# Kernel optimization log

Hardware: AMD Instinct MI355X
Metric: run time of the kernel (lower is better)

Reference implementation:

```python
import jax, jax.numpy as jnp
import numpy as np

C = 128          # channels per irrep
N = 16000        # nodes (atoms)
E = 256000       # edges (neighbour pairs)
A = 10           # node attribute (species) dim, '10x0e'
RB = 8           # radial basis features
H = 64           # radial MLP hidden width
INV_SQRT3 = 0.5773502691896258  # normalised CG for 1o x 1o -> 0e


def setup_inputs() -> dict:
    key = jax.random.key(0)
    ks = jax.random.split(key, 16)
    s = lambda fan: 1.0  # weights ~ N(0,1); e3nn-style 1/sqrt(fan_in) applied in forward
    return {
        "node_features": jax.random.normal(ks[0], (N, 4 * C), jnp.float32),   # [N, 128x0e + 128x1o]
        "node_attributes": jax.random.uniform(ks[1], (N, A), jnp.float32),
        "sph_harmonics": jax.random.normal(ks[2], (E, 4), jnp.float32),        # [E, 0e(1)+1o(3)]
        "radial_basis": jax.random.normal(ks[3], (E, RB), jnp.float32),
        "edge_index": jax.random.randint(ks[4], (2, E), 0, N),                 # [senders; receivers]
        # pre_linear (per-irrep channel mixing)
        "Wpre0": jax.random.normal(ks[5], (C, C), jnp.float32),
        "Wpre1": jax.random.normal(ks[6], (C, C), jnp.float32),
        # radial MLP 8 -> 64 -> 64 -> weight_numel(=4*C), no bias
        "Wm1": jax.random.normal(ks[7], (RB, H), jnp.float32),
        "Wm2": jax.random.normal(ks[8], (H, H), jnp.float32),
        "Wm3": jax.random.normal(ks[9], (H, 4 * C), jnp.float32),
        # post_linear: mid irreps 256x0e + 256x1o -> 128x0e + 128x1o
        "Wpost0": jax.random.normal(ks[10], (2 * C, C), jnp.float32),
        "Wpost1": jax.random.normal(ks[11], (2 * C, C), jnp.float32),
        # attribute mixer: FullyConnectedTensorProduct(features_out, '10x0e', features_out)
        "Wa0": jax.random.normal(ks[12], (C, A, C), jnp.float32),
        "Wa1": jax.random.normal(ks[13], (C, A, C), jnp.float32),
    }


def reference(node_features, node_attributes, sph_harmonics, radial_basis, edge_index,
              Wpre0, Wpre1, Wm1, Wm2, Wm3, Wpost0, Wpost1, Wa0, Wa1):
    n = node_features.shape[0]
    inv_c = 1.0 / np.sqrt(C).astype(np.float32)
    inv_2c = 1.0 / np.sqrt(2 * C).astype(np.float32)
    inv_ca = 1.0 / np.sqrt(C * A).astype(np.float32)

    # split e3nn-layout features: scalars [N,C], vectors [N,C,3]
    x0 = node_features[:, :C]
    x1 = node_features[:, C:].reshape(n, C, 3)

    # pre_linear (o3.Linear: per-irrep channel mix, 1/sqrt(fan_in))
    h0 = (x0 @ Wpre0) * inv_c
    h1 = jnp.einsum('nud,uw->nwd', x1, Wpre1) * inv_c

    snd, rcv = edge_index[0], edge_index[1]
    e0 = h0[snd]            # [E,C]   gather neighbour scalars
    e1 = h1[snd]            # [E,C,3] gather neighbour vectors
    Y0 = sph_harmonics[:, :1]   # [E,1]
    Y1 = sph_harmonics[:, 1:]   # [E,3]

    # per-edge TP weights from radial MLP (SiLU, no bias)
    hmlp = jax.nn.silu(radial_basis @ Wm1)
    hmlp = jax.nn.silu(hmlp @ Wm2)
    w = (hmlp @ Wm3).reshape(-1, 4, C)  # [E,4,C], one weight per (path, channel)

    # channel-wise (uvu) tensor product, CG-sparse paths:
    m0a = w[:, 0] * e0 * Y0                                              # 0e x 0e -> 0e
    m0b = w[:, 1] * jnp.einsum('ecd,ed->ec', e1, Y1) * INV_SQRT3         # 1o x 1o -> 0e
    m1a = w[:, 2][:, :, None] * e0[:, :, None] * Y1[:, None, :]          # 0e x 1o -> 1o
    m1b = w[:, 3][:, :, None] * e1 * Y0[:, :, None]                      # 1o x 0e -> 1o

    M0 = jnp.concatenate([m0a, m0b], axis=1)   # [E,2C]  mid 256x0e
    M1 = jnp.concatenate([m1a, m1b], axis=1)   # [E,2C,3] mid 256x1o

    # scatter-sum aggregation onto receiving nodes
    A0 = jax.ops.segment_sum(M0, rcv, num_segments=n)
    A1 = jax.ops.segment_sum(M1, rcv, num_segments=n)

    # post_linear: 256x0e+256x1o -> 128x0e+128x1o
    o0 = (A0 @ Wpost0) * inv_2c
    o1 = jnp.einsum('nud,uw->nwd', A1, Wpost1) * inv_2c

    # attribute mixer: FCTP with '10x0e' (scalars mix channels per irrep)
    a0 = jnp.einsum('nu,nv,uvw->nw', o0, node_attributes, Wa0) * inv_ca
    a1 = jnp.einsum('nud,nv,uvw->nwd', o1, node_attributes, Wa1) * inv_ca

    # UnflattenIrreps: [N, channels, irreps_dim] with dims 0e(1)+1o(3)
    return jnp.concatenate([a0[:, :, None], a1], axis=2)  # [N, C, 4]
```

## Files before the change

### kernel.cpp

```cpp
#include <hip/hip_runtime.h>
#include <hip/hip_bf16.h>

#define NN 16000
#define CC 128
#define EE 256000
#define AA 10

typedef short short8_t __attribute__((ext_vector_type(8)));
typedef float f32x4 __attribute__((ext_vector_type(4)));
typedef unsigned short u16x4 __attribute__((ext_vector_type(4)));

__device__ __forceinline__ float silu_f(float x) {
    return x / (1.0f + __expf(-x));
}

__device__ __forceinline__ float bf2f(unsigned short u) {
    unsigned int x = ((unsigned int)u) << 16;
    float f;
    __builtin_memcpy(&f, &x, 4);
    return f;
}

__device__ __forceinline__ unsigned short f2bf(float f) {
    __hip_bfloat16 b = __float2bfloat16(f);
    unsigned short u;
    __builtin_memcpy(&u, &b, 2);
    return u;
}

__global__ __launch_bounds__(256) void pre_kernel(const float* __restrict__ nf,
                                                  const float* __restrict__ Wpre0,
                                                  const float* __restrict__ Wpre1,
                                                  float4* __restrict__ h4) {
    __shared__ float4 lx[2][CC];
    const int c = threadIdx.x & 127;
    const int sub = threadIdx.x >> 7;
    const float inv_c = 0.08838834764831843f;
    const int n = blockIdx.x * 2 + sub;
    const float* row = nf + (size_t)n * 512;
    lx[sub][c] = make_float4(row[c], row[128 + 3 * c], row[128 + 3 * c + 1], row[128 + 3 * c + 2]);
    __syncthreads();
    float4 acc = make_float4(0.f, 0.f, 0.f, 0.f);
    #pragma unroll 8
    for (int u = 0; u < 128; ++u) {
        const float w0 = Wpre0[u * 128 + c];
        const float w1 = Wpre1[u * 128 + c];
        const float4 xv = lx[sub][u];
        acc.x += w0 * xv.x;
        acc.y += w1 * xv.y;
        acc.z += w1 * xv.z;
        acc.w += w1 * xv.w;
    }
    acc.x *= inv_c; acc.y *= inv_c; acc.z *= inv_c; acc.w *= inv_c;
    h4[(size_t)n * 128 + c] = acc;
}

__global__ __launch_bounds__(256) void count_kernel(const int* __restrict__ ei,
                                                    int* __restrict__ cnt) {
    const int e = blockIdx.x * 256 + threadIdx.x;
    if (e < EE) atomicAdd(&cnt[ei[EE + e]], 1);
}

__global__ __launch_bounds__(1024) void scan_kernel(const int* __restrict__ cnt,
                                                    int* __restrict__ cur) {
    __shared__ int part[1024];
    const int t = threadIdx.x;
    const int base = t * 16;
    int local[16];
    int s = 0;
    #pragma unroll
    for (int i = 0; i < 16; ++i) {
        const int idx = base + i;
        const int v = (idx < NN) ? cnt[idx] : 0;
        local[i] = s;
        s += v;
    }
    part[t] = s;
    __syncthreads();
    for (int off = 1; off < 1024; off <<= 1) {
        int v = (t >= off) ? part[t - off] : 0;
        __syncthreads();
        part[t] += v;
        __syncthreads();
    }
    const int pre = (t == 0) ? 0 : part[t - 1];
    #pragma unroll
    for (int i = 0; i < 16; ++i) {
        const int idx = base + i;
        if (idx < NN) cur[idx] = pre + local[i];
    }
}

__global__ __launch_bounds__(256) void fill_kernel(const int* __restrict__ ei,
                                                   int* __restrict__ cur,
                                                   int* __restrict__ perm) {
    const int e = blockIdx.x * 256 + threadIdx.x;
    if (e < EE) {
        const int r = ei[EE + e];
        const int pos = atomicAdd(&cur[r], 1);
        perm[pos] = e;
    }
}

__global__ __launch_bounds__(256) void gather_kernel(const int* __restrict__ perm,
                                                     const int* __restrict__ ei,
                                                     const float4* __restrict__ sph4,
                                                     int* __restrict__ ss,
                                                     int* __restrict__ rs,
                                                     float4* __restrict__ Ys) {
    const int e = blockIdx.x * 256 + threadIdx.x;
    const int p = perm[e];
    ss[e] = ei[p];
    rs[e] = ei[EE + p];
    Ys[e] = sph4[p];
}

__global__ __launch_bounds__(256) void mlp_kernel(const float* __restrict__ rb,
                                                  const float* __restrict__ Wm1,
                                                  const float* __restrict__ Wm2,
                                                  const int* __restrict__ perm,
                                                  unsigned short* __restrict__ hmS) {
    __shared__ float4 sW1[8][16];
    __shared__ float4 sW2[64][16];
    __shared__ unsigned short sH[256][64];
    const int tid = threadIdx.x;
    for (int i = tid; i < 8 * 16; i += 256) ((float4*)sW1)[i] = ((const float4*)Wm1)[i];
    for (int i = tid; i < 64 * 16; i += 256) ((float4*)sW2)[i] = ((const float4*)Wm2)[i];
    __syncthreads();
    const int e = blockIdx.x * 256 + tid;
    const int p = perm[e];
    const float4* rb4 = (const float4*)(rb + (size_t)p * 8);
    const float4 r0 = rb4[0], r1 = rb4[1];
    float r[8] = {r0.x, r0.y, r0.z, r0.w, r1.x, r1.y, r1.z, r1.w};
    float h1[64];
    #pragma unroll
    for (int o4 = 0; o4 < 16; ++o4) {
        float4 a = make_float4(0.f, 0.f, 0.f, 0.f);
        #pragma unroll
        for (int k = 0; k < 8; ++k) {
            const float4 wv = sW1[k][o4];
            a.x += r[k] * wv.x; a.y += r[k] * wv.y; a.z += r[k] * wv.z; a.w += r[k] * wv.w;
        }
        h1[o4 * 4 + 0] = silu_f(a.x);
        h1[o4 * 4 + 1] = silu_f(a.y);
        h1[o4 * 4 + 2] = silu_f(a.z);
        h1[o4 * 4 + 3] = silu_f(a.w);
    }
    #pragma unroll
    for (int o4 = 0; o4 < 16; ++o4) {
        float4 a = make_float4(0.f, 0.f, 0.f, 0.f);
        #pragma unroll 8
        for (int k = 0; k < 64; ++k) {
            const float4 wv = sW2[k][o4];
            a.x += h1[k] * wv.x; a.y += h1[k] * wv.y; a.z += h1[k] * wv.z; a.w += h1[k] * wv.w;
        }
        sH[tid][o4 * 4 + 0] = f2bf(silu_f(a.x));
        sH[tid][o4 * 4 + 1] = f2bf(silu_f(a.y));
        sH[tid][o4 * 4 + 2] = f2bf(silu_f(a.z));
        sH[tid][o4 * 4 + 3] = f2bf(silu_f(a.w));
    }
    __syncthreads();
    uint4* g4 = (uint4*)(hmS + (size_t)blockIdx.x * 256 * 64);
    const uint4* s4 = (const uint4*)sH;
    for (int i = tid; i < 2048; i += 256) g4[i] = s4[i];
}

__global__ __launch_bounds__(256) void w3t_kernel(const float* __restrict__ Wm3,
                                                  unsigned short* __restrict__ W3Thi,
                                                  unsigned short* __restrict__ W3Tlo) {
    const int idx = blockIdx.x * 256 + threadIdx.x;
    const int col = idx >> 6, k = idx & 63;
    const float v = Wm3[k * 512 + col];
    const unsigned short hi = f2bf(v);
    W3Thi[idx] = hi;
    W3Tlo[idx] = f2bf(v - bf2f(hi));
}

__global__ __launch_bounds__(512) void wmsgm_kernel(const unsigned short* __restrict__ hmS,
                                                    const unsigned short* __restrict__ W3Thi,
                                                    const unsigned short* __restrict__ W3Tlo,
                                                    const int* __restrict__ ss,
                                                    const int* __restrict__ rs,
                                                    const float4* __restrict__ Ys,
                                                    const float4* __restrict__ h4,
                                                    float* __restrict__ Acat) {
    __shared__ int lss[64];
    __shared__ int lrs[64];
    __shared__ float4 lY[64];
    const int tid = threadIdx.x;
    const int ebase = blockIdx.x * 64;
    if (tid < 64) {
        lss[tid] = ss[ebase + tid];
        lrs[tid] = rs[ebase + tid];
        lY[tid] = Ys[ebase + tid];
    }
    const int w = tid >> 6, lane = tid & 63;
    const int l15 = lane & 15, lk = lane >> 4;

    f32x4 acc[4][4];
    #pragma unroll
    for (int mf = 0; mf < 4; ++mf)
        #pragma unroll
        for (int g = 0; g < 4; ++g) acc[mf][g] = (f32x4){0.f, 0.f, 0.f, 0.f};

    #pragma unroll
    for (int pass = 0; pass < 2; ++pass) {
        const unsigned short* W3T = pass == 0 ? W3Thi : W3Tlo;
        short8_t b[4][2];
        #pragma unroll
        for (int g = 0; g < 4; ++g)
            #pragma unroll
            for (int ks = 0; ks < 2; ++ks)
                b[g][ks] = *(const short8_t*)&W3T[(size_t)(g * 128 + w * 16 + l15) * 64 + ks * 32 + lk * 8];
        #pragma unroll
        for (int mf = 0; mf < 4; ++mf) {
            const int erow = 16 * (l15 >> 2) + 4 * mf + (l15 & 3);
            const size_t rowb = (size_t)(ebase + erow) * 64;
            const short8_t a0 = *(const short8_t*)&hmS[rowb + lk * 8];
            const short8_t a1 = *(const short8_t*)&hmS[rowb + 32 + lk * 8];
            #pragma unroll
            for (int g = 0; g < 4; ++g) {
                acc[mf][g] = __builtin_amdgcn_mfma_f32_16x16x32_bf16(a0, b[g][0], acc[mf][g], 0, 0, 0);
                acc[mf][g] = __builtin_amdgcn_mfma_f32_16x16x32_bf16(a1, b[g][1], acc[mf][g], 0, 0, 0);
            }
        }
    }
    __syncthreads();

    const int cidx = w * 16 + l15;
    float s0 = 0.f, s1 = 0.f, s2 = 0.f, s3 = 0.f, s4v = 0.f, s5 = 0.f, s6 = 0.f, s7 = 0.f;
    int cr = lrs[lk * 16];
    #pragma unroll
    for (int mf = 0; mf < 4; ++mf) {
        #pragma unroll
        for (int reg = 0; reg < 4; ++reg) {
            const int el = lk * 16 + mf * 4 + reg;
            const int r = lrs[el];
            if (r != cr) {
                float* arow = Acat + (size_t)cr * 1024;
                atomicAdd(arow + cidx, s0);
                atomicAdd(arow + 128 + cidx, s1);
                atomicAdd(arow + 256 + cidx, s2);
                atomicAdd(arow + 512 + cidx, s3);
                atomicAdd(arow + 768 + cidx, s4v);
                atomicAdd(arow + 384 + cidx, s5);
                atomicAdd(arow + 640 + cidx, s6);
                atomicAdd(arow + 896 + cidx, s7);
                s0 = s1 = s2 = s3 = s4v = s5 = s6 = s7 = 0.f;
                cr = r;
            }
            const float4 Y = lY[el];
            const float4 hv = h4[(size_t)lss[el] * 128 + cidx];
            const float w0 = acc[mf][0][reg];
            const float w1 = acc[mf][1][reg];
            const float w2 = acc[mf][2][reg];
            const float w3 = acc[mf][3][reg];
            s0 += w0 * hv.x * Y.x;
            s1 += w1 * (hv.y * Y.y + hv.z * Y.z + hv.w * Y.w) * 0.5773502691896258f;
            const float m = w2 * hv.x;
            s2 += m * Y.y; s3 += m * Y.z; s4v += m * Y.w;
            const float m2 = w3 * Y.x;
            s5 += m2 * hv.y; s6 += m2 * hv.z; s7 += m2 * hv.w;
        }
    }
    {
        float* arow = Acat + (size_t)cr * 1024;
        atomicAdd(arow + cidx, s0);
        atomicAdd(arow + 128 + cidx, s1);
        atomicAdd(arow + 256 + cidx, s2);
        atomicAdd(arow + 512 + cidx, s3);
        atomicAdd(arow + 768 + cidx, s4v);
        atomicAdd(arow + 384 + cidx, s5);
        atomicAdd(arow + 640 + cidx, s6);
        atomicAdd(arow + 896 + cidx, s7);
    }
}

__global__ __launch_bounds__(256) void posto_kernel(const float* __restrict__ Acat,
                                                    const float* __restrict__ Wpost0,
                                                    const float* __restrict__ Wpost1,
                                                    float* __restrict__ o) {
    __shared__ float sA[4][256][16];
    const int tid = threadIdx.x;
    const int nb = blockIdx.x * 16;
    {
        const int n = tid & 15, idx = tid >> 4;
        const float4* row4 = (const float4*)(Acat + (size_t)(nb + n) * 1024);
        #pragma unroll
        for (int rr = 0; rr < 16; ++rr) {
            const int f4 = idx + rr * 16;
            const float4 v = row4[f4];
            const int flat = f4 * 4;
            const int d = flat >> 8;
            const int u = flat & 255;
            sA[d][u + 0][n] = v.x;
            sA[d][u + 1][n] = v.y;
            sA[d][u + 2][n] = v.z;
            sA[d][u + 3][n] = v.w;
        }
    }
    __syncthreads();
    const int c = tid & 127, half = tid >> 7, dlo = half * 2;
    const float* W0 = (half == 0) ? Wpost0 : Wpost1;
    float acc0[16], acc1[16];
    #pragma unroll
    for (int n = 0; n < 16; ++n) { acc0[n] = 0.f; acc1[n] = 0.f; }
    #pragma unroll 2
    for (int u = 0; u < 256; ++u) {
        const float w0 = W0[u * 128 + c];
        const float w1 = Wpost1[u * 128 + c];
        #pragma unroll
        for (int n = 0; n < 16; ++n) {
            acc0[n] += sA[dlo][u][n] * w0;
            acc1[n] += sA[dlo + 1][u][n] * w1;
        }
    }
    const float inv_2c = 0.0625f;
    #pragma unroll
    for (int n = 0; n < 16; ++n) {
        o[((size_t)(nb + n) * 4 + dlo) * 128 + c] = acc0[n] * inv_2c;
        o[((size_t)(nb + n) * 4 + dlo + 1) * 128 + c] = acc1[n] * inv_2c;
    }
}

__global__ __launch_bounds__(256) void watT_kernel(const float* __restrict__ Wa0,
                                                   const float* __restrict__ Wa1,
                                                   unsigned short* __restrict__ WaT) {
    __shared__ unsigned short tile[128][129];
    const int tid = threadIdx.x;
    const int v = blockIdx.x;
    const int arr = blockIdx.y;
    const float* Wa = (arr == 0) ? Wa0 : Wa1;
    {
        const int u = tid >> 1, half = tid & 1;
        const float4* src = (const float4*)(Wa + ((size_t)u * AA + v) * 128 + half * 64);
        #pragma unroll
        for (int j = 0; j < 16; ++j) {
            const float4 val = src[j];
            const int w = half * 64 + j * 4;
            tile[w + 0][u] = f2bf(val.x);
            tile[w + 1][u] = f2bf(val.y);
            tile[w + 2][u] = f2bf(val.z);
            tile[w + 3][u] = f2bf(val.w);
        }
    }
    __syncthreads();
    {
        const int w = tid >> 1, half = tid & 1;
        unsigned short* dst = WaT + (size_t)arr * 163840 + (size_t)v * 16384 + (size_t)w * 128;
        #pragma unroll
        for (int j = 0; j < 8; ++j) {
            const int u0 = half * 64 + j * 8;
            union { unsigned short s[8]; uint4 q; } pk;
            #pragma unroll
            for (int k = 0; k < 8; ++k) pk.s[k] = tile[w][u0 + k];
            *(uint4*)(dst + u0) = pk.q;
        }
    }
}

__global__ __launch_bounds__(256) void attrm_kernel(const float* __restrict__ o,
                                                    const float* __restrict__ attr,
                                                    const unsigned short* __restrict__ WaT,
                                                    float* __restrict__ tmp) {
    __shared__ unsigned short sA[128][128];
    __shared__ unsigned short sB[128][128];
    __shared__ float sat[128][AA];
    const int tid = threadIdx.x;
    const int d = blockIdx.y;
    const int nb = blockIdx.x * 128;
    const unsigned short* Wp = WaT + (d == 0 ? 0 : 163840);

    {
        const int n = tid >> 1, half = tid & 1;
        const float4* src = (const float4*)(o + ((size_t)(nb + n) * 4 + d) * 128 + half * 64);
        #pragma unroll
        for (int j = 0; j < 16; ++j) {
            const float4 val = src[j];
            const int u0 = (half * 64 + j * 4) ^ ((n & 7) << 3);
            u16x4 pk;
            pk.x = f2bf(val.x); pk.y = f2bf(val.y); pk.z = f2bf(val.z); pk.w = f2bf(val.w);
            *(u16x4*)&sA[n][u0] = pk;
        }
    }
    for (int i = tid; i < 128 * AA; i += 256) ((float*)sat)[i] = attr[(size_t)nb * AA + i];

    const int wid = tid >> 6, lane = tid & 63;
    const int wr = wid >> 1, wc = wid & 1;
    const int lrow = lane & 15, lk = lane >> 4;

    f32x4 tot[4][4];
    #pragma unroll
    for (int mf = 0; mf < 4; ++mf)
        #pragma unroll
        for (int cf = 0; cf < 4; ++cf) tot[mf][cf] = (f32x4){0.f, 0.f, 0.f, 0.f};

    for (int v = 0; v < AA; ++v) {
        __syncthreads();
        {
            const uint4* src = (const uint4*)(Wp + (size_t)v * 16384);
            #pragma unroll
            for (int j = 0; j < 8; ++j) {
                const int cidx = tid + j * 256;
                const int w = cidx >> 4;
                const int u0 = ((cidx & 15) * 8) ^ ((w & 7) << 3);
                const uint4 val = src[cidx];
                *(uint4*)&sB[w][u0] = val;
            }
        }
        __syncthreads();

        f32x4 acc[4][4];
        #pragma unroll
        for (int mf = 0; mf < 4; ++mf)
            #pragma unroll
            for (int cf = 0; cf < 4; ++cf) acc[mf][cf] = (f32x4){0.f, 0.f, 0.f, 0.f};

        #pragma unroll
        for (int ks = 0; ks < 4; ++ks) {
            const int ku = ks * 32 + lk * 8;
            short8_t a[4], b[4];
            #pragma unroll
            for (int mf = 0; mf < 4; ++mf) {
                const int row = wr * 64 + mf * 16 + lrow;
                a[mf] = *(const short8_t*)&sA[row][ku ^ ((row & 7) << 3)];
            }
            #pragma unroll
            for (int cf = 0; cf < 4; ++cf) {
                const int col = wc * 64 + cf * 16 + lrow;
                b[cf] = *(const short8_t*)&sB[col][ku ^ ((col & 7) << 3)];
            }
            #pragma unroll
            for (int mf = 0; mf < 4; ++mf)
                #pragma unroll
                for (int cf = 0; cf < 4; ++cf)
                    acc[mf][cf] = __builtin_amdgcn_mfma_f32_16x16x32_bf16(a[mf], b[cf], acc[mf][cf], 0, 0, 0);
        }

        #pragma unroll
        for (int mf = 0; mf < 4; ++mf) {
            const int row0 = wr * 64 + mf * 16 + lk * 4;
            #pragma unroll
            for (int j = 0; j < 4; ++j) {
                const float wj = sat[row0 + j][v];
                #pragma unroll
                for (int cf = 0; cf < 4; ++cf)
                    tot[mf][cf][j] += wj * acc[mf][cf][j];
            }
        }
    }

    const float inv_ca = 0.027950849718747373f;
    #pragma unroll
    for (int mf = 0; mf < 4; ++mf) {
        #pragma unroll
        for (int j = 0; j < 4; ++j) {
            const int n = nb + wr * 64 + mf * 16 + lk * 4 + j;
            #pragma unroll
            for (int cf = 0; cf < 4; ++cf) {
                const int col = wc * 64 + cf * 16 + lrow;
                tmp[(size_t)d * 2048000 + (size_t)n * 128 + col] = tot[mf][cf][j] * inv_ca;
            }
        }
    }
}

__global__ __launch_bounds__(256) void pack_kernel(const float* __restrict__ tmp,
                                                   float4* __restrict__ out4) {
    const size_t e = (size_t)blockIdx.x * 256 + threadIdx.x;
    out4[e] = make_float4(tmp[e], tmp[2048000 + e], tmp[4096000 + e], tmp[6144000 + e]);
}

extern "C" void kernel_launch(void* const* d_in, const int* in_sizes, int n_in,
                              void* d_out, int out_size, void* d_ws, size_t ws_size,
                              hipStream_t stream) {
    const float* nf    = (const float*)d_in[0];
    const float* attr  = (const float*)d_in[1];
    const float* sph   = (const float*)d_in[2];
    const float* rb    = (const float*)d_in[3];
    const int*   ei    = (const int*)d_in[4];
    const float* Wpre0 = (const float*)d_in[5];
    const float* Wpre1 = (const float*)d_in[6];
    const float* Wm1   = (const float*)d_in[7];
    const float* Wm2   = (const float*)d_in[8];
    const float* Wm3   = (const float*)d_in[9];
    const float* Wpost0= (const float*)d_in[10];
    const float* Wpost1= (const float*)d_in[11];
    const float* Wa0   = (const float*)d_in[12];
    const float* Wa1   = (const float*)d_in[13];
    float* out = (float*)d_out;

    float* ws = (float*)d_ws;
    float4* h4 = (float4*)ws;
    unsigned short* hmS = (unsigned short*)(ws + (size_t)8192000);
    float* Acat = ws + (size_t)16384000;
    int* perm = (int*)(Acat + (size_t)16384000);
    int* cur  = perm + 256000;
    int* cnt  = cur + 16384;
    int* ss   = cnt + 16384;
    int* rs   = ss + 256000;
    float4* Ys = (float4*)(rs + 256000);
    unsigned short* W3Thi = (unsigned short*)perm;
    unsigned short* W3Tlo = W3Thi + 32768;
    float* o = ws;
    float* tmp = Acat;
    unsigned short* WaT = (unsigned short*)(Acat + (size_t)8192000);

    hipMemsetAsync(Acat, 0, (size_t)NN * 1024 * sizeof(float), stream);
    hipMemsetAsync(cnt, 0, 16384 * sizeof(int), stream);

    pre_kernel<<<NN / 2, 256, 0, stream>>>(nf, Wpre0, Wpre1, h4);
    count_kernel<<<EE / 256, 256, 0, stream>>>(ei, cnt);
    scan_kernel<<<1, 1024, 0, stream>>>(cnt, cur);
    fill_kernel<<<EE / 256, 256, 0, stream>>>(ei, cur, perm);
    gather_kernel<<<EE / 256, 256, 0, stream>>>(perm, ei, (const float4*)sph, ss, rs, Ys);
    mlp_kernel<<<EE / 256, 256, 0, stream>>>(rb, Wm1, Wm2, perm, hmS);
    w3t_kernel<<<128, 256, 0, stream>>>(Wm3, W3Thi, W3Tlo);
    wmsgm_kernel<<<EE / 64, 512, 0, stream>>>(hmS, W3Thi, W3Tlo, ss, rs, Ys, h4, Acat);
    posto_kernel<<<NN / 16, 256, 0, stream>>>(Acat, Wpost0, Wpost1, o);
    watT_kernel<<<dim3(AA, 2), 256, 0, stream>>>(Wa0, Wa1, WaT);
    attrm_kernel<<<dim3(NN / 128, 4), 256, 0, stream>>>(o, attr, WaT, tmp);
    pack_kernel<<<8000, 256, 0, stream>>>(tmp, (float4*)out);
}
```

Measured before the change: 716.4 us.

## Move post-linear GEMM to bf16 MFMA with split hi/lo precision emulation

Replaces the scalar-FMA post_linear kernel with an MFMA-based GEMM over 128-node tiles per irrep component. It uses a three-term bf16 split (A_hi*W_hi, A_hi*W_lo, A_lo*W_hi) to approximate fp32 accuracy, and stages an XOR-swizzled shared tile. This targets the FP32 ALU cost of the 16000x256x128 products. In exchange it repeatedly converts Wpost from global memory inside the inner loop and drops the lo*lo term, which slightly reduces accuracy.

```diff
diff --git a/kernel.cpp b/kernel.cpp
--- a/kernel.cpp
+++ b/kernel.cpp
@@ -276,50 +276,95 @@
     }
 }
 
-__global__ __launch_bounds__(256) void posto_kernel(const float* __restrict__ Acat,
-                                                    const float* __restrict__ Wpost0,
-                                                    const float* __restrict__ Wpost1,
-                                                    float* __restrict__ o) {
-    __shared__ float sA[4][256][16];
+__global__ __launch_bounds__(256) void postom_kernel(const float* __restrict__ Acat,
+                                                     const float* __restrict__ Wpost0,
+                                                     const float* __restrict__ Wpost1,
+                                                     float* __restrict__ o) {
+    __shared__ unsigned short sA[128][256];
     const int tid = threadIdx.x;
-    const int nb = blockIdx.x * 16;
-    {
-        const int n = tid & 15, idx = tid >> 4;
-        const float4* row4 = (const float4*)(Acat + (size_t)(nb + n) * 1024);
-        #pragma unroll
-        for (int rr = 0; rr < 16; ++rr) {
-            const int f4 = idx + rr * 16;
-            const float4 v = row4[f4];
-            const int flat = f4 * 4;
-            const int d = flat >> 8;
-            const int u = flat & 255;
-            sA[d][u + 0][n] = v.x;
-            sA[d][u + 1][n] = v.y;
-            sA[d][u + 2][n] = v.z;
-            sA[d][u + 3][n] = v.w;
-        }
-    }
-    __syncthreads();
-    const int c = tid & 127, half = tid >> 7, dlo = half * 2;
-    const float* W0 = (half == 0) ? Wpost0 : Wpost1;
-    float acc0[16], acc1[16];
-    #pragma unroll
-    for (int n = 0; n < 16; ++n) { acc0[n] = 0.f; acc1[n] = 0.f; }
-    #pragma unroll 2
-    for (int u = 0; u < 256; ++u) {
-        const float w0 = W0[u * 128 + c];
-        const float w1 = Wpost1[u * 128 + c];
-        #pragma unroll
-        for (int n = 0; n < 16; ++n) {
-            acc0[n] += sA[dlo][u][n] * w0;
-            acc1[n] += sA[dlo + 1][u][n] * w1;
-        }
-    }
+    const int d = blockIdx.y;
+    const int nb = blockIdx.x * 128;
+    const float* Wp = (d == 0) ? Wpost0 : Wpost1;
+
+    const int wid = tid >> 6, lane = tid & 63;
+    const int wr = wid >> 1, wc = wid & 1;
+    const int l15 = lane & 15, lk = lane >> 4;
+
+    f32x4 acc[4][4];
+    #pragma unroll
+    for (int mf = 0; mf < 4; ++mf)
+        #pragma unroll
+        for (int cf = 0; cf < 4; ++cf) acc[mf][cf] = (f32x4){0.f, 0.f, 0.f, 0.f};
+
+    #pragma unroll
+    for (int pass = 0; pass < 2; ++pass) {
+        __syncthreads();
+        {
+            const int n = tid >> 1, half = tid & 1;
+            const float4* src = (const float4*)(Acat + (size_t)(nb + n) * 1024 + (d << 8)) + half * 32;
+            #pragma unroll
+            for (int j = 0; j < 32; j += 2) {
+                const float4 v0 = src[j];
+                const float4 v1 = src[j + 1];
+                const int k0 = (half * 128 + j * 4) ^ ((n & 7) << 3);
+                union { unsigned short s[8]; uint4 q; } pk;
+                const float f0[8] = {v0.x, v0.y, v0.z, v0.w, v1.x, v1.y, v1.z, v1.w};
+                #pragma unroll
+                for (int q = 0; q < 8; ++q) {
+                    const unsigned short hi = f2bf(f0[q]);
+                    pk.s[q] = (pass == 0) ? hi : f2bf(f0[q] - bf2f(hi));
+                }
+                *(uint4*)&sA[n][k0] = pk.q;
+            }
+        }
+        __syncthreads();
+
+        #pragma unroll
+        for (int ks = 0; ks < 8; ++ks) {
+            const int ku = ks * 32 + lk * 8;
+            short8_t a[4];
+            #pragma unroll
+            for (int mf = 0; mf < 4; ++mf) {
+                const int row = wr * 64 + mf * 16 + l15;
+                a[mf] = *(const short8_t*)&sA[row][ku ^ ((row & 7) << 3)];
+            }
+            short8_t bh[4], bl[4];
+            #pragma unroll
+            for (int cf = 0; cf < 4; ++cf) {
+                const int col = wc * 64 + cf * 16 + l15;
+                union { unsigned short s[8]; short8_t v; } h, l;
+                #pragma unroll
+                for (int q = 0; q < 8; ++q) {
+                    const float f = Wp[(size_t)(ku + q) * 128 + col];
+                    const unsigned short hi = f2bf(f);
+                    h.s[q] = hi;
+                    l.s[q] = f2bf(f - bf2f(hi));
+                }
+                bh[cf] = h.v; bl[cf] = l.v;
+            }
+            #pragma unroll
+            for (int mf = 0; mf < 4; ++mf)
+                #pragma unroll
+                for (int cf = 0; cf < 4; ++cf) {
+                    acc[mf][cf] = __builtin_amdgcn_mfma_f32_16x16x32_bf16(a[mf], bh[cf], acc[mf][cf], 0, 0, 0);
+                    if (pass == 0)
+                        acc[mf][cf] = __builtin_amdgcn_mfma_f32_16x16x32_bf16(a[mf], bl[cf], acc[mf][cf], 0, 0, 0);
+                }
+        }
+    }
+
     const float inv_2c = 0.0625f;
     #pragma unroll
-    for (int n = 0; n < 16; ++n) {
-        o[((size_t)(nb + n) * 4 + dlo) * 128 + c] = acc0[n] * inv_2c;
-        o[((size_t)(nb + n) * 4 + dlo + 1) * 128 + c] = acc1[n] * inv_2c;
+    for (int mf = 0; mf < 4; ++mf) {
+        #pragma unroll
+        for (int j = 0; j < 4; ++j) {
+            const int n = nb + wr * 64 + mf * 16 + lk * 4 + j;
+            #pragma unroll
+            for (int cf = 0; cf < 4; ++cf) {
+                const int col = wc * 64 + cf * 16 + l15;
+                o[((size_t)n * 4 + d) * 128 + col] = acc[mf][cf][j] * inv_2c;
+            }
+        }
     }
 }
 
@@ -517,7 +562,7 @@
     mlp_kernel<<<EE / 256, 256, 0, stream>>>(rb, Wm1, Wm2, perm, hmS);
     w3t_kernel<<<128, 256, 0, stream>>>(Wm3, W3Thi, W3Tlo);
     wmsgm_kernel<<<EE / 64, 512, 0, stream>>>(hmS, W3Thi, W3Tlo, ss, rs, Ys, h4, Acat);
-    posto_kernel<<<NN / 16, 256, 0, stream>>>(Acat, Wpost0, Wpost1, o);
+    postom_kernel<<<dim3(NN / 128, 4), 256, 0, stream>>>(Acat, Wpost0, Wpost1, o);
     watT_kernel<<<dim3(AA, 2), 256, 0, stream>>>(Wa0, Wa1, WaT);
     attrm_kernel<<<dim3(NN / 128, 4), 256, 0, stream>>>(o, attr, WaT, tmp);
     pack_kernel<<<8000, 256, 0, stream>>>(tmp, (float4*)out);
```

Result: faster. 669.1 us (-6.6%).
